# Kernel optimization log

Hardware: AMD Instinct MI355X
Metric: run time of the kernel (lower is better)

Reference implementation:

```python
import jax, jax.numpy as jnp
import numpy as np

N, T, E, A, D, O, S, R = 64, 1000, 512, 256, 256, 80, 64, 2
ATT_RANGE = 10
H = 4 * D  # LSTM hidden size = 1024
K = 31     # location conv kernel width


def setup_inputs() -> dict:
    key = jax.random.key(0)
    ks = jax.random.split(key, 16)
    def rn(k, shape, scale=0.05):
        return (jax.random.normal(k, shape) * scale).astype(jnp.float32)
    return {
        "input_enc": jax.random.normal(ks[0], (N, T, E), jnp.float32),
        "input_dec": jax.random.normal(ks[1], (N, O), jnp.float32),
        "spkr_vec": jax.random.normal(ks[2], (N, 1, S), jnp.float32),
        "lengths_enc": jnp.full((N,), T, dtype=jnp.int32),
        "w_enc": rn(ks[3], (E, A)), "b_enc": jnp.zeros((A,), jnp.float32),
        "w_spkr": rn(ks[4], (S, A)),
        "conv_w": rn(ks[5], (A, 1, K)),
        "w_proj": rn(ks[6], (A, 1)), "b_proj": jnp.zeros((1,), jnp.float32),
        "w_p1": rn(ks[7], (O + S, 2 * D)), "b_p1": jnp.zeros((2 * D,), jnp.float32),
        "w_p2": rn(ks[8], (2 * D, D)), "b_p2": jnp.zeros((D,), jnp.float32),
        "w_ih0": rn(ks[9], (E + D + S, 4 * H)), "w_hh0": rn(ks[10], (H, 4 * H)),
        "b_ih0": jnp.zeros((4 * H,), jnp.float32), "b_hh0": jnp.zeros((4 * H,), jnp.float32),
        "w_ih1": rn(ks[11], (H, 4 * H)), "w_hh1": rn(ks[12], (H, 4 * H)),
        "b_ih1": jnp.zeros((4 * H,), jnp.float32), "b_hh1": jnp.zeros((4 * H,), jnp.float32),
        "w_out": rn(ks[13], (E + H, O * R)), "b_out": jnp.zeros((O * R,), jnp.float32),
    }


def _softsign(x):
    return x / (1.0 + jnp.abs(x))


def _lstm_cell_zero_state(x, w_ih, b_ih, b_hh):
    # h0 = c0 = 0, so the w_hh contribution vanishes on the first step
    gates = x @ w_ih + b_ih + b_hh          # [N, 4H]
    i, f, g, o = jnp.split(gates, 4, axis=-1)  # torch gate order i,f,g,o
    c = jax.nn.sigmoid(i) * jnp.tanh(g)
    return jax.nn.sigmoid(o) * jnp.tanh(c)


def reference(input_enc, input_dec, spkr_vec, lengths_enc,
              w_enc, b_enc, w_spkr, conv_w, w_proj, b_proj,
              w_p1, b_p1, w_p2, b_p2,
              w_ih0, w_hh0, b_ih0, b_hh0, w_ih1, w_hh1, b_ih1, b_hh1,
              w_out, b_out):
    n, t_enc, _ = input_enc.shape
    # initial attention weights: one-hot at t=0 (null_state branch)
    a0 = jnp.zeros((n, t_enc), input_enc.dtype).at[:, 0].set(1.0)

    bias_enc = _softsign(input_enc @ w_enc + b_enc)   # [N, T, A]
    bias_spkr = _softsign(spkr_vec @ w_spkr)          # [N, 1, A] broadcast

    # location features: conv1d over prev attention, padding 15, no bias
    prev_feat = jax.lax.conv_general_dilated(
        a0[:, None, :], conv_w, (1,), [(K // 2, K // 2)],
        dimension_numbers=("NCH", "OIH", "NCH"))    # [N, A, T]
    prev_feat = prev_feat.transpose(0, 2, 1)          # [N, T, A]

    # hidden is None on the first step -> in_att_dec = 0
    e = bias_enc + bias_spkr + prev_feat              # [N, T, A]

    # windowed attention mask around argmax of previous weights (no grad)
    max_idx = jnp.argmax(a0, axis=1)                  # [N]
    lim = jnp.maximum(lengths_enc.astype(jnp.int32) - 1, 0)  # [N]
    offs = jnp.arange(ATT_RANGE, dtype=jnp.int32)
    idx1 = jnp.minimum(jnp.maximum(max_idx[:, None] + offs, 0), lim[:, None])
    idx2 = jnp.minimum(jnp.maximum(max_idx[:, None] - offs, 0), lim[:, None])
    idxs = jnp.concatenate([idx1, idx2], axis=1)      # [N, 2*ATT_RANGE]
    rows = jnp.arange(n)[:, None]
    att_mask = jnp.zeros((n, t_enc), e.dtype).at[rows, idxs].set(1.0)
    att_mask = jax.lax.stop_gradient(att_mask)

    logit = (jnp.tanh(e) @ w_proj + b_proj)[..., 0]   # [N, T]
    logit = logit - jnp.max(logit, axis=1, keepdims=True)
    w = jnp.exp(logit) * att_mask
    att = w / jnp.maximum(jnp.sum(w, axis=1, keepdims=True), 1e-12)  # F.normalize p=1

    context = jnp.einsum("nt,nte->ne", att, input_enc)  # [N, E]

    # prenet (dropout in eval mode = identity)
    spkr = spkr_vec[:, 0, :]
    pre = jnp.concatenate([input_dec, spkr], axis=-1)
    pre = jax.nn.relu(pre @ w_p1 + b_p1)
    pre = jax.nn.relu(pre @ w_p2 + b_p2)               # [N, D]

    x = jnp.concatenate([pre, context, spkr], axis=-1)  # [N, D+E+S]
    h1 = _lstm_cell_zero_state(x, w_ih0, b_ih0, b_hh0)   # [N, H]
    h2 = _lstm_cell_zero_state(h1, w_ih1, b_ih1, b_hh1)  # [N, H]
    _ = (w_hh0, w_hh1)  # recurrent weights unused on first step (zero state)

    dec = jnp.concatenate([h2, context], axis=-1)        # [N, H+E]
    out = (dec @ w_out + b_out).reshape(n, R, O)         # [N, r_factor, O]
    return out
```

## Files before the change

### kernel.cpp

```cpp
#include <hip/hip_runtime.h>
#include <hip/hip_bf16.h>
#include <math.h>

#define N_   64
#define T_   1000
#define E_   512
#define A_   256
#define O_   80
#define S_   64
#define H_   1024
#define G4_  4096
#define KC_  31

__device__ __forceinline__ float sigmoidf_(float x) { return 1.f / (1.f + __expf(-x)); }
__device__ __forceinline__ float softsignf_(float x) { return x / (1.f + fabsf(x)); }

__global__ __launch_bounds__(512) void logits_kernel(
    const float* __restrict__ enc,
    const float* __restrict__ spkr,
    const float* __restrict__ w_enc,
    const float* __restrict__ b_enc,
    const float* __restrict__ w_spkr,
    const float* __restrict__ conv_w,
    const float* __restrict__ w_proj,
    float* __restrict__ part) {
  int n  = blockIdx.x;
  int aq = blockIdx.y;
  int tid = threadIdx.x;
  int al = tid & 63;
  int kw = tid >> 6;
  int a  = aq * 64 + al;

  __shared__ float smem[5120];
  __shared__ float sp[S_];
  __shared__ float bsl[S_];

  if (tid < S_) sp[tid] = spkr[n * S_ + tid];
  {
    const float4* src = (const float4*)(enc + (size_t)n * T_ * E_);
    float4* dst = (float4*)smem;
    for (int i = tid; i < 1280; i += 512) dst[i] = src[i];
  }
  __syncthreads();

  if (tid < S_) {
    float b = 0.f;
    #pragma unroll 8
    for (int s = 0; s < S_; ++s) b += sp[s] * w_spkr[s * A_ + aq * 64 + tid];
    bsl[tid] = softsignf_(b);
  }

  float acc[10];
  #pragma unroll
  for (int t = 0; t < 10; ++t) acc[t] = 0.f;
  const int kbase = kw * 64;
  const float* wcol = w_enc + a;
  #pragma unroll 8
  for (int k = 0; k < 64; ++k) {
    float we = wcol[(size_t)(kbase + k) * A_];
    #pragma unroll
    for (int t = 0; t < 10; ++t)
      acc[t] = fmaf(smem[t * E_ + kbase + k], we, acc[t]);
  }

  __syncthreads();
  #pragma unroll
  for (int t = 0; t < 10; ++t) smem[(kw * 10 + t) * 64 + al] = acc[t];
  __syncthreads();

  #pragma unroll
  for (int tb = 0; tb < 10; tb += 8) {
    int t = tb + kw;
    if (t < 10 && (tb == 0 || kw < 2)) {
      float p = b_enc[a];
      #pragma unroll
      for (int w = 0; w < 8; ++w) p += smem[(w * 10 + t) * 64 + al];
      float e = softsignf_(p) + bsl[al] + conv_w[a * KC_ + (15 - t)];
      float l = tanhf(e) * w_proj[a];
      #pragma unroll
      for (int off = 32; off > 0; off >>= 1) l += __shfl_down(l, off);
      if (al == 0) part[(n * 10 + t) * 4 + aq] = l;
    }
  }
}

__global__ __launch_bounds__(512) void ctx_prenet_kernel(
    const float* __restrict__ enc,
    const float* __restrict__ dec_in,
    const float* __restrict__ spkr,
    const int*   __restrict__ lengths,
    const float* __restrict__ part,
    const float* __restrict__ w_p1,
    const float* __restrict__ b_p1,
    const float* __restrict__ w_p2,
    const float* __restrict__ b_p2,
    float* __restrict__ xbuf) {
  int n = blockIdx.x;
  int tid = threadIdx.x;
  __shared__ float att[10];
  __shared__ float incat[O_ + S_];
  __shared__ float pre1[512];
  __shared__ float pp2[2][A_];

  if (tid < S_) {
    float s = spkr[n * S_ + tid];
    incat[O_ + tid] = s;
    xbuf[n * 832 + 768 + tid] = s;
  }
  if (tid < O_) incat[tid] = dec_in[n * O_ + tid];
  if (tid == 0) {
    int lim = lengths[n] - 1; if (lim < 0) lim = 0;
    int tmax = lim < 9 ? lim : 9;
    float lg[10];
    float m = -1e30f;
    for (int t = 0; t <= tmax; ++t) {
      const float* p = &part[(n * 10 + t) * 4];
      lg[t] = p[0] + p[1] + p[2] + p[3];
      m = fmaxf(m, lg[t]);
    }
    float ssum = 0.f;
    for (int t = 0; t <= tmax; ++t) { float w = __expf(lg[t] - m); att[t] = w; ssum += w; }
    float inv = 1.f / fmaxf(ssum, 1e-12f);
    for (int t = 0; t <= tmax; ++t) att[t] *= inv;
    for (int t = tmax + 1; t < 10; ++t) att[t] = 0.f;
  }
  __syncthreads();

  {
    float c = 0.f;
    #pragma unroll
    for (int t = 0; t < 10; ++t)
      c = fmaf(att[t], enc[(size_t)n * T_ * E_ + t * E_ + tid], c);
    xbuf[n * 832 + 256 + tid] = c;
  }

  {
    float v = b_p1[tid];
    #pragma unroll 8
    for (int k = 0; k < O_ + S_; ++k) v = fmaf(incat[k], w_p1[k * 512 + tid], v);
    pre1[tid] = fmaxf(v, 0.f);
  }
  __syncthreads();

  {
    int c  = tid & 255;
    int kh = tid >> 8;
    float v = 0.f;
    #pragma unroll 8
    for (int k = kh * 256; k < kh * 256 + 256; ++k)
      v = fmaf(pre1[k], w_p2[k * A_ + c], v);
    pp2[kh][c] = v;
  }
  __syncthreads();
  if (tid < A_) {
    float v = b_p2[tid] + pp2[0][tid] + pp2[1][tid];
    xbuf[n * 832 + tid] = fmaxf(v, 0.f);
  }
}

__global__ __launch_bounds__(512) void gemm_gates_kernel(
    const float* __restrict__ X, int ldx, int K,
    const float* __restrict__ W,
    const float* __restrict__ b1,
    const float* __restrict__ b2,
    float* __restrict__ G) {
  int bt = blockIdx.x;
  int c0 = bt * 16; if (c0 >= 1024) c0 += 1024;
  int tid = threadIdx.x;
  int kh  = tid >> 8;
  int lt  = tid & 255;
  int tr  = lt >> 4;
  int tc  = lt & 15;
  int c   = c0 + tc;
  int Kh  = K >> 1;
  int kbeg = kh * Kh;
  int NC  = Kh >> 5;

  int rr  = lt & 63;
  int kb8 = (lt >> 6) << 3;

  __shared__ float xs[2][2][32][64];
  __shared__ float red[16][16][4];

  const float* xsrc = X + (size_t)rr * ldx + kbeg + kb8;

  float4 xv0 = ((const float4*)xsrc)[0];
  float4 xv1 = ((const float4*)(xsrc + 4))[0];
  {
    float* d = &xs[kh][0][kb8][rr];
    d[0]   = xv0.x; d[64]  = xv0.y; d[128] = xv0.z; d[192] = xv0.w;
    d[256] = xv1.x; d[320] = xv1.y; d[384] = xv1.z; d[448] = xv1.w;
  }
  __syncthreads();

  float acc0 = 0.f, acc1 = 0.f, acc2 = 0.f, acc3 = 0.f;
  for (int ch = 0; ch < NC; ++ch) {
    int buf = ch & 1;
    float wreg[32];
    const float* wp = W + (size_t)(kbeg + ch * 32) * G4_ + c;
    #pragma unroll
    for (int kk = 0; kk < 32; ++kk) wreg[kk] = wp[(size_t)kk * G4_];
    bool more = (ch + 1 < NC);
    if (more) {
      const float* s = xsrc + (ch + 1) * 32;
      xv0 = ((const float4*)s)[0];
      xv1 = ((const float4*)(s + 4))[0];
    }
    const float* xb = &xs[kh][buf][0][tr * 4];
    #pragma unroll
    for (int kk = 0; kk < 32; ++kk) {
      float4 xv = *(const float4*)(xb + kk * 64);
      acc0 = fmaf(xv.x, wreg[kk], acc0);
      acc1 = fmaf(xv.y, wreg[kk], acc1);
      acc2 = fmaf(xv.z, wreg[kk], acc2);
      acc3 = fmaf(xv.w, wreg[kk], acc3);
    }
    if (more) {
      float* d = &xs[kh][buf ^ 1][kb8][rr];
      d[0]   = xv0.x; d[64]  = xv0.y; d[128] = xv0.z; d[192] = xv0.w;
      d[256] = xv1.x; d[320] = xv1.y; d[384] = xv1.z; d[448] = xv1.w;
    }
    __syncthreads();
  }

  if (kh == 1) {
    red[tr][tc][0] = acc0; red[tr][tc][1] = acc1;
    red[tr][tc][2] = acc2; red[tr][tc][3] = acc3;
  }
  __syncthreads();
  if (kh == 0) {
    float bb = b1[c] + b2[c];
    int r = tr * 4;
    G[(size_t)(r + 0) * G4_ + c] = acc0 + red[tr][tc][0] + bb;
    G[(size_t)(r + 1) * G4_ + c] = acc1 + red[tr][tc][1] + bb;
    G[(size_t)(r + 2) * G4_ + c] = acc2 + red[tr][tc][2] + bb;
    G[(size_t)(r + 3) * G4_ + c] = acc3 + red[tr][tc][3] + bb;
  }
}

__global__ void lstm_act_kernel(const float* __restrict__ G, float* __restrict__ H) {
  int idx = blockIdx.x * 256 + threadIdx.x;
  int n = idx >> 10;
  int j = idx & 1023;
  float gi = G[(size_t)n * G4_ + j];
  float gg = G[(size_t)n * G4_ + 2048 + j];
  float go = G[(size_t)n * G4_ + 3072 + j];
  float cc = sigmoidf_(gi) * tanhf(gg);
  H[n * H_ + j] = sigmoidf_(go) * tanhf(cc);
}

__global__ __launch_bounds__(1024) void out_kernel(
    const float* __restrict__ G1,
    const float* __restrict__ xbuf,
    const float* __restrict__ w_out,
    const float* __restrict__ b_out,
    float* __restrict__ out) {
  int n = blockIdx.x;
  int tid = threadIdx.x;
  __shared__ float dl[1536];
  __shared__ float pp[6][160];
  {
    float gi = G1[(size_t)n * G4_ + tid];
    float gg = G1[(size_t)n * G4_ + 2048 + tid];
    float go = G1[(size_t)n * G4_ + 3072 + tid];
    dl[tid] = sigmoidf_(go) * tanhf(sigmoidf_(gi) * tanhf(gg));
  }
  if (tid < E_) dl[1024 + tid] = xbuf[n * 832 + 256 + tid];
  __syncthreads();
  if (tid < 960) {
    int c  = tid % 160;
    int kq = tid / 160;
    float acc = 0.f;
    const float* wp = w_out + (size_t)(kq * 256) * 160 + c;
    const float* dp = dl + kq * 256;
    #pragma unroll 8
    for (int k = 0; k < 256; ++k) acc = fmaf(dp[k], wp[(size_t)k * 160], acc);
    pp[kq][c] = acc;
  }
  __syncthreads();
  if (tid < 160) {
    float r = b_out[tid] + pp[0][tid] + pp[1][tid] + pp[2][tid]
            + pp[3][tid] + pp[4][tid] + pp[5][tid];
    out[n * 160 + tid] = r;
  }
}

extern "C" void kernel_launch(void* const* d_in, const int* in_sizes, int n_in,
                              void* d_out, int out_size, void* d_ws, size_t ws_size,
                              hipStream_t stream) {
  const float* input_enc = (const float*)d_in[0];
  const float* input_dec = (const float*)d_in[1];
  const float* spkr_vec  = (const float*)d_in[2];
  const int*   lengths   = (const int*)  d_in[3];
  const float* w_enc     = (const float*)d_in[4];
  const float* b_enc     = (const float*)d_in[5];
  const float* w_spkr    = (const float*)d_in[6];
  const float* conv_w    = (const float*)d_in[7];
  const float* w_proj    = (const float*)d_in[8];
  const float* w_p1      = (const float*)d_in[10];
  const float* b_p1      = (const float*)d_in[11];
  const float* w_p2      = (const float*)d_in[12];
  const float* b_p2      = (const float*)d_in[13];
  const float* w_ih0     = (const float*)d_in[14];
  const float* b_ih0     = (const float*)d_in[16];
  const float* b_hh0     = (const float*)d_in[17];
  const float* w_ih1     = (const float*)d_in[18];
  const float* b_ih1     = (const float*)d_in[20];
  const float* b_hh1     = (const float*)d_in[21];
  const float* w_out     = (const float*)d_in[22];
  const float* b_out     = (const float*)d_in[23];

  float* ws    = (float*)d_ws;
  float* part  = ws;
  float* xbuf  = ws + 4096;
  float* gates = ws + 65536;
  float* h1    = ws + 327680;
  float* out   = (float*)d_out;

  hipLaunchKernelGGL(logits_kernel, dim3(64, 4), dim3(512), 0, stream,
                     input_enc, spkr_vec, w_enc, b_enc, w_spkr, conv_w, w_proj, part);
  hipLaunchKernelGGL(ctx_prenet_kernel, dim3(64), dim3(512), 0, stream,
                     input_enc, input_dec, spkr_vec, lengths, part,
                     w_p1, b_p1, w_p2, b_p2, xbuf);
  hipLaunchKernelGGL(gemm_gates_kernel, dim3(192), dim3(512), 0, stream,
                     xbuf, 832, 832, w_ih0, b_ih0, b_hh0, gates);
  hipLaunchKernelGGL(lstm_act_kernel, dim3(256), dim3(256), 0, stream, gates, h1);
  hipLaunchKernelGGL(gemm_gates_kernel, dim3(192), dim3(512), 0, stream,
                     h1, 1024, 1024, w_ih1, b_ih1, b_hh1, gates);
  hipLaunchKernelGGL(out_kernel, dim3(64), dim3(1024), 0, stream,
                     gates, xbuf, w_out, b_out, out);
}
```

Measured before the change: 98.70 us.

## Fuse LSTM activation into gate GEMM and batch rows in output projection

The gate GEMM now computes the i, g and o gate columns for 8 hidden units per block, reduces them in shared memory and applies the LSTM activation directly. This removes the separate activation kernel and the round trip of the full gate matrix through global memory. The output kernel now reads the precomputed h2 and processes 8 batch rows per block over a 20-column slice, so each w_out element fetched is reused across those 8 rows. In exchange, blocks are larger (768 threads), there are fewer of them (128), and only part of the threads load X tiles.

```diff
diff --git a/kernel.cpp b/kernel.cpp
--- a/kernel.cpp
+++ b/kernel.cpp
@@ -158,35 +158,38 @@
   }
 }
 
-__global__ __launch_bounds__(512) void gemm_gates_kernel(
+__global__ __launch_bounds__(768) void gemm_gates_act_kernel(
     const float* __restrict__ X, int ldx, int K,
     const float* __restrict__ W,
     const float* __restrict__ b1,
     const float* __restrict__ b2,
-    float* __restrict__ G) {
-  int bt = blockIdx.x;
-  int c0 = bt * 16; if (c0 >= 1024) c0 += 1024;
+    float* __restrict__ H) {
+  int j0 = blockIdx.x * 8;
   int tid = threadIdx.x;
-  int kh  = tid >> 8;
-  int lt  = tid & 255;
-  int tr  = lt >> 4;
-  int tc  = lt & 15;
-  int c   = c0 + tc;
+  int kh  = tid / 384;
+  int r   = tid % 384;
+  int tr  = r / 24;
+  int tc  = r % 24;
+  int col = (tc < 8) ? (j0 + tc) : ((tc < 16) ? (2048 + j0 + tc - 8)
+                                              : (3072 + j0 + tc - 16));
   int Kh  = K >> 1;
   int kbeg = kh * Kh;
   int NC  = Kh >> 5;
 
-  int rr  = lt & 63;
-  int kb8 = (lt >> 6) << 3;
+  bool st = (r < 256);
+  int rr  = r & 63;
+  int kb8 = (r >> 6) << 3;
 
   __shared__ float xs[2][2][32][64];
-  __shared__ float red[16][16][4];
+  __shared__ float red[16][24][4];
+  __shared__ float gsum[64][25];
 
   const float* xsrc = X + (size_t)rr * ldx + kbeg + kb8;
 
-  float4 xv0 = ((const float4*)xsrc)[0];
-  float4 xv1 = ((const float4*)(xsrc + 4))[0];
-  {
+  float4 xv0, xv1;
+  if (st) {
+    xv0 = ((const float4*)xsrc)[0];
+    xv1 = ((const float4*)(xsrc + 4))[0];
     float* d = &xs[kh][0][kb8][rr];
     d[0]   = xv0.x; d[64]  = xv0.y; d[128] = xv0.z; d[192] = xv0.w;
     d[256] = xv1.x; d[320] = xv1.y; d[384] = xv1.z; d[448] = xv1.w;
@@ -197,11 +200,11 @@
   for (int ch = 0; ch < NC; ++ch) {
     int buf = ch & 1;
     float wreg[32];
-    const float* wp = W + (size_t)(kbeg + ch * 32) * G4_ + c;
+    const float* wp = W + (size_t)(kbeg + ch * 32) * G4_ + col;
     #pragma unroll
     for (int kk = 0; kk < 32; ++kk) wreg[kk] = wp[(size_t)kk * G4_];
     bool more = (ch + 1 < NC);
-    if (more) {
+    if (st && more) {
       const float* s = xsrc + (ch + 1) * 32;
       xv0 = ((const float4*)s)[0];
       xv1 = ((const float4*)(s + 4))[0];
@@ -215,7 +218,7 @@
       acc2 = fmaf(xv.z, wreg[kk], acc2);
       acc3 = fmaf(xv.w, wreg[kk], acc3);
     }
-    if (more) {
+    if (st && more) {
       float* d = &xs[kh][buf ^ 1][kb8][rr];
       d[0]   = xv0.x; d[64]  = xv0.y; d[128] = xv0.z; d[192] = xv0.w;
       d[256] = xv1.x; d[320] = xv1.y; d[384] = xv1.z; d[448] = xv1.w;
@@ -229,59 +232,64 @@
   }
   __syncthreads();
   if (kh == 0) {
-    float bb = b1[c] + b2[c];
-    int r = tr * 4;
-    G[(size_t)(r + 0) * G4_ + c] = acc0 + red[tr][tc][0] + bb;
-    G[(size_t)(r + 1) * G4_ + c] = acc1 + red[tr][tc][1] + bb;
-    G[(size_t)(r + 2) * G4_ + c] = acc2 + red[tr][tc][2] + bb;
-    G[(size_t)(r + 3) * G4_ + c] = acc3 + red[tr][tc][3] + bb;
-  }
-}
-
-__global__ void lstm_act_kernel(const float* __restrict__ G, float* __restrict__ H) {
-  int idx = blockIdx.x * 256 + threadIdx.x;
-  int n = idx >> 10;
-  int j = idx & 1023;
-  float gi = G[(size_t)n * G4_ + j];
-  float gg = G[(size_t)n * G4_ + 2048 + j];
-  float go = G[(size_t)n * G4_ + 3072 + j];
-  float cc = sigmoidf_(gi) * tanhf(gg);
-  H[n * H_ + j] = sigmoidf_(go) * tanhf(cc);
-}
-
-__global__ __launch_bounds__(1024) void out_kernel(
-    const float* __restrict__ G1,
+    float bb = b1[col] + b2[col];
+    int rbase = tr * 4;
+    gsum[rbase + 0][tc] = acc0 + red[tr][tc][0] + bb;
+    gsum[rbase + 1][tc] = acc1 + red[tr][tc][1] + bb;
+    gsum[rbase + 2][tc] = acc2 + red[tr][tc][2] + bb;
+    gsum[rbase + 3][tc] = acc3 + red[tr][tc][3] + bb;
+  }
+  __syncthreads();
+  if (tid < 512) {
+    int n  = tid >> 3;
+    int jj = tid & 7;
+    float gi = gsum[n][jj];
+    float gg = gsum[n][8 + jj];
+    float go = gsum[n][16 + jj];
+    H[(size_t)n * H_ + j0 + jj] = sigmoidf_(go) * tanhf(sigmoidf_(gi) * tanhf(gg));
+  }
+}
+
+#define DLP 1544
+__global__ __launch_bounds__(512) void out_kernel(
+    const float* __restrict__ h2,
     const float* __restrict__ xbuf,
     const float* __restrict__ w_out,
     const float* __restrict__ b_out,
     float* __restrict__ out) {
-  int n = blockIdx.x;
+  int bn = blockIdx.x >> 3;
+  int c0 = (blockIdx.x & 7) * 20;
   int tid = threadIdx.x;
-  __shared__ float dl[1536];
-  __shared__ float pp[6][160];
-  {
-    float gi = G1[(size_t)n * G4_ + tid];
-    float gg = G1[(size_t)n * G4_ + 2048 + tid];
-    float go = G1[(size_t)n * G4_ + 3072 + tid];
-    dl[tid] = sigmoidf_(go) * tanhf(sigmoidf_(gi) * tanhf(gg));
-  }
-  if (tid < E_) dl[1024 + tid] = xbuf[n * 832 + 256 + tid];
-  __syncthreads();
-  if (tid < 960) {
-    int c  = tid % 160;
+  __shared__ float dl[8][DLP];
+  __shared__ float pp[3][160];
+
+  for (int idx = tid; idx < 8 * 1536; idx += 512) {
+    int nl = idx / 1536;
+    int k  = idx % 1536;
+    int n  = bn * 8 + nl;
+    dl[nl][k] = (k < 1024) ? h2[(size_t)n * H_ + k]
+                           : xbuf[n * 832 + 256 + (k - 1024)];
+  }
+  __syncthreads();
+
+  if (tid < 480) {
     int kq = tid / 160;
+    int o  = tid % 160;
+    int nl = o / 20;
+    int cl = o % 20;
+    const float* wp = w_out + (size_t)(kq * 512) * 160 + c0 + cl;
+    const float* dp = &dl[nl][kq * 512];
     float acc = 0.f;
-    const float* wp = w_out + (size_t)(kq * 256) * 160 + c;
-    const float* dp = dl + kq * 256;
     #pragma unroll 8
-    for (int k = 0; k < 256; ++k) acc = fmaf(dp[k], wp[(size_t)k * 160], acc);
-    pp[kq][c] = acc;
+    for (int k = 0; k < 512; ++k) acc = fmaf(dp[k], wp[(size_t)k * 160], acc);
+    pp[kq][o] = acc;
   }
   __syncthreads();
   if (tid < 160) {
-    float r = b_out[tid] + pp[0][tid] + pp[1][tid] + pp[2][tid]
-            + pp[3][tid] + pp[4][tid] + pp[5][tid];
-    out[n * 160 + tid] = r;
+    int nl = tid / 20;
+    int cl = tid % 20;
+    float v = b_out[c0 + cl] + pp[0][tid] + pp[1][tid] + pp[2][tid];
+    out[(size_t)(bn * 8 + nl) * 160 + c0 + cl] = v;
   }
 }
 
@@ -313,8 +321,8 @@
   float* ws    = (float*)d_ws;
   float* part  = ws;
   float* xbuf  = ws + 4096;
-  float* gates = ws + 65536;
-  float* h1    = ws + 327680;
+  float* h1    = ws + 65536;
+  float* h2    = ws + 131072;
   float* out   = (float*)d_out;
 
   hipLaunchKernelGGL(logits_kernel, dim3(64, 4), dim3(512), 0, stream,
@@ -322,11 +330,10 @@
   hipLaunchKernelGGL(ctx_prenet_kernel, dim3(64), dim3(512), 0, stream,
                      input_enc, input_dec, spkr_vec, lengths, part,
                      w_p1, b_p1, w_p2, b_p2, xbuf);
-  hipLaunchKernelGGL(gemm_gates_kernel, dim3(192), dim3(512), 0, stream,
-                     xbuf, 832, 832, w_ih0, b_ih0, b_hh0, gates);
-  hipLaunchKernelGGL(lstm_act_kernel, dim3(256), dim3(256), 0, stream, gates, h1);
-  hipLaunchKernelGGL(gemm_gates_kernel, dim3(192), dim3(512), 0, stream,
-                     h1, 1024, 1024, w_ih1, b_ih1, b_hh1, gates);
-  hipLaunchKernelGGL(out_kernel, dim3(64), dim3(1024), 0, stream,
-                     gates, xbuf, w_out, b_out, out);
-}
+  hipLaunchKernelGGL(gemm_gates_act_kernel, dim3(128), dim3(768), 0, stream,
+                     xbuf, 832, 832, w_ih0, b_ih0, b_hh0, h1);
+  hipLaunchKernelGGL(gemm_gates_act_kernel, dim3(128), dim3(768), 0, stream,
+                     h1, 1024, 1024, w_ih1, b_ih1, b_hh1, h2);
+  hipLaunchKernelGGL(out_kernel, dim3(64), dim3(512), 0, stream,
+                     h2, xbuf, w_out, b_out, out);
+}
```

New measurement: 381.5 us. 3.87x slower.

## Stage gate-GEMM weights through LDS and retile output projection by batch groups

Applied to the files above, without the earlier changes.

In the gate GEMM, each thread used to load its own 32 weight values per chunk directly from global memory, and 16 threads of a row group read the same column. Weights are now loaded cooperatively, two values per thread, into a double-buffered LDS tile alongside the activations, which reduces redundant global traffic. The output kernel is retiled so each block handles 8 batch rows by 20 output columns with a 3-way K split. Each block now recomputes the LSTM activations for its 8 rows, so that work is repeated 8 times across the column blocks, and the block uses more shared memory.

```diff
diff --git a/kernel.cpp b/kernel.cpp
--- a/kernel.cpp
+++ b/kernel.cpp
@@ -178,47 +178,58 @@
 
   int rr  = lt & 63;
   int kb8 = (lt >> 6) << 3;
+  int wr  = lt >> 4;
+  int wc  = lt & 15;
 
   __shared__ float xs[2][2][32][64];
+  __shared__ float wsl[2][2][32][16];
   __shared__ float red[16][16][4];
 
   const float* xsrc = X + (size_t)rr * ldx + kbeg + kb8;
+  const float* wsrc = W + (size_t)(kbeg + wr) * G4_ + c0 + wc;
 
   float4 xv0 = ((const float4*)xsrc)[0];
   float4 xv1 = ((const float4*)(xsrc + 4))[0];
+  float  wv0 = wsrc[0];
+  float  wv1 = wsrc[(size_t)16 * G4_];
   {
     float* d = &xs[kh][0][kb8][rr];
     d[0]   = xv0.x; d[64]  = xv0.y; d[128] = xv0.z; d[192] = xv0.w;
     d[256] = xv1.x; d[320] = xv1.y; d[384] = xv1.z; d[448] = xv1.w;
+    wsl[kh][0][wr][wc]      = wv0;
+    wsl[kh][0][wr + 16][wc] = wv1;
   }
   __syncthreads();
 
   float acc0 = 0.f, acc1 = 0.f, acc2 = 0.f, acc3 = 0.f;
   for (int ch = 0; ch < NC; ++ch) {
     int buf = ch & 1;
-    float wreg[32];
-    const float* wp = W + (size_t)(kbeg + ch * 32) * G4_ + c;
-    #pragma unroll
-    for (int kk = 0; kk < 32; ++kk) wreg[kk] = wp[(size_t)kk * G4_];
     bool more = (ch + 1 < NC);
     if (more) {
       const float* s = xsrc + (ch + 1) * 32;
       xv0 = ((const float4*)s)[0];
       xv1 = ((const float4*)(s + 4))[0];
+      const float* wsp = wsrc + (size_t)(ch + 1) * 32 * G4_;
+      wv0 = wsp[0];
+      wv1 = wsp[(size_t)16 * G4_];
     }
     const float* xb = &xs[kh][buf][0][tr * 4];
+    const float* wb = &wsl[kh][buf][0][tc];
     #pragma unroll
     for (int kk = 0; kk < 32; ++kk) {
+      float w = wb[kk * 16];
       float4 xv = *(const float4*)(xb + kk * 64);
-      acc0 = fmaf(xv.x, wreg[kk], acc0);
-      acc1 = fmaf(xv.y, wreg[kk], acc1);
-      acc2 = fmaf(xv.z, wreg[kk], acc2);
-      acc3 = fmaf(xv.w, wreg[kk], acc3);
+      acc0 = fmaf(xv.x, w, acc0);
+      acc1 = fmaf(xv.y, w, acc1);
+      acc2 = fmaf(xv.z, w, acc2);
+      acc3 = fmaf(xv.w, w, acc3);
     }
     if (more) {
       float* d = &xs[kh][buf ^ 1][kb8][rr];
       d[0]   = xv0.x; d[64]  = xv0.y; d[128] = xv0.z; d[192] = xv0.w;
       d[256] = xv1.x; d[320] = xv1.y; d[384] = xv1.z; d[448] = xv1.w;
+      wsl[kh][buf ^ 1][wr][wc]      = wv0;
+      wsl[kh][buf ^ 1][wr + 16][wc] = wv1;
     }
     __syncthreads();
   }
@@ -249,39 +260,52 @@
   H[n * H_ + j] = sigmoidf_(go) * tanhf(cc);
 }
 
-__global__ __launch_bounds__(1024) void out_kernel(
-    const float* __restrict__ G1,
+#define DLP 1544
+__global__ __launch_bounds__(512) void out_kernel(
+    const float* __restrict__ gates,
     const float* __restrict__ xbuf,
     const float* __restrict__ w_out,
     const float* __restrict__ b_out,
     float* __restrict__ out) {
-  int n = blockIdx.x;
+  int bn = blockIdx.x >> 3;
+  int c0 = (blockIdx.x & 7) * 20;
   int tid = threadIdx.x;
-  __shared__ float dl[1536];
-  __shared__ float pp[6][160];
-  {
-    float gi = G1[(size_t)n * G4_ + tid];
-    float gg = G1[(size_t)n * G4_ + 2048 + tid];
-    float go = G1[(size_t)n * G4_ + 3072 + tid];
-    dl[tid] = sigmoidf_(go) * tanhf(sigmoidf_(gi) * tanhf(gg));
-  }
-  if (tid < E_) dl[1024 + tid] = xbuf[n * 832 + 256 + tid];
-  __syncthreads();
-  if (tid < 960) {
-    int c  = tid % 160;
+  __shared__ float dl[8][DLP];
+  __shared__ float pp[3][160];
+
+  for (int idx = tid; idx < 8 * 1536; idx += 512) {
+    int nl = idx / 1536;
+    int k  = idx % 1536;
+    int n  = bn * 8 + nl;
+    if (k < 1024) {
+      float gi = gates[(size_t)n * G4_ + k];
+      float gg = gates[(size_t)n * G4_ + 2048 + k];
+      float go = gates[(size_t)n * G4_ + 3072 + k];
+      dl[nl][k] = sigmoidf_(go) * tanhf(sigmoidf_(gi) * tanhf(gg));
+    } else {
+      dl[nl][k] = xbuf[n * 832 + 256 + (k - 1024)];
+    }
+  }
+  __syncthreads();
+
+  if (tid < 480) {
     int kq = tid / 160;
+    int o  = tid % 160;
+    int nl = o / 20;
+    int cl = o % 20;
+    const float* wp = w_out + (size_t)(kq * 512) * 160 + c0 + cl;
+    const float* dp = &dl[nl][kq * 512];
     float acc = 0.f;
-    const float* wp = w_out + (size_t)(kq * 256) * 160 + c;
-    const float* dp = dl + kq * 256;
     #pragma unroll 8
-    for (int k = 0; k < 256; ++k) acc = fmaf(dp[k], wp[(size_t)k * 160], acc);
-    pp[kq][c] = acc;
+    for (int k = 0; k < 512; ++k) acc = fmaf(dp[k], wp[(size_t)k * 160], acc);
+    pp[kq][o] = acc;
   }
   __syncthreads();
   if (tid < 160) {
-    float r = b_out[tid] + pp[0][tid] + pp[1][tid] + pp[2][tid]
-            + pp[3][tid] + pp[4][tid] + pp[5][tid];
-    out[n * 160 + tid] = r;
+    int nl = tid / 20;
+    int cl = tid % 20;
+    float v = b_out[c0 + cl] + pp[0][tid] + pp[1][tid] + pp[2][tid];
+    out[(size_t)(bn * 8 + nl) * 160 + c0 + cl] = v;
   }
 }
 
@@ -327,6 +351,6 @@
   hipLaunchKernelGGL(lstm_act_kernel, dim3(256), dim3(256), 0, stream, gates, h1);
   hipLaunchKernelGGL(gemm_gates_kernel, dim3(192), dim3(512), 0, stream,
                      h1, 1024, 1024, w_ih1, b_ih1, b_hh1, gates);
-  hipLaunchKernelGGL(out_kernel, dim3(64), dim3(1024), 0, stream,
+  hipLaunchKernelGGL(out_kernel, dim3(64), dim3(512), 0, stream,
                      gates, xbuf, w_out, b_out, out);
 }
```

Result: slower. 106.0 us (+7.4%).
